# Performance work log

Hardware: AMD Instinct MI355X
Metric: run time of the kernel (lower is better)

## Reference

```python
import jax, jax.numpy as jnp
import numpy as np

B, L, D = 32, 4096, 1024

def setup_inputs() -> dict:
    key = jax.random.key(0)
    k1, k2, k3, k4 = jax.random.split(key, 4)
    doc_rep = jax.random.normal(k1, (B, L, D), dtype=jnp.float32)
    # cls_layer: Linear(input_size=D, label_size=L) -> weight [L, D], bias [L]
    W = jax.random.normal(k2, (L, D), dtype=jnp.float32) / np.sqrt(D)
    b = jax.random.normal(k3, (L,), dtype=jnp.float32) * 0.01
    # label_graph initialized as identity + learned; use identity + small noise-free eye
    G = jnp.eye(L, dtype=jnp.float32)
    return {"doc_rep": doc_rep, "W": W, "b": b, "G": G}

def reference(doc_rep, W, b, G):
    # Original computes full [B, L, L] = Linear(doc_rep) then extracts the diagonal.
    # Mathematically only the per-label dot products are needed:
    # doc_label[b, l] = doc_rep[b, l, :] @ W[l, :] + bias[l]
    doc_label = jnp.einsum('bld,ld->bl', doc_rep, W) + b  # [B, L]
    out_label = jax.nn.sigmoid(doc_label @ G)             # [B, L]
    return out_label
```

## Files before the change

### kernel.cpp

```cpp
#include <hip/hip_runtime.h>
#include <math.h>

#define BB 32
#define LL 4096
#define DD 1024
#define NCH 16
#define NJT 64
#define CTILE 256

typedef float f4 __attribute__((ext_vector_type(4)));

__global__ __launch_bounds__(256, 8) void k_dot(const float* __restrict__ doc,
                                                const float* __restrict__ W,
                                                const float* __restrict__ bias,
                                                float* __restrict__ dlT) {
  const int bid  = (blockIdx.x & 7) * 2048 + (blockIdx.x >> 3);
  const int wid  = (bid * 256 + (int)threadIdx.x) >> 6;
  const int lane = threadIdx.x & 63;
  const int b  = wid & 31;
  const int l  = (wid >> 5) << 1;

  const f4* dp = reinterpret_cast<const f4*>(doc) +
                 (((size_t)b << 20) + ((size_t)l << 8));
  const f4* wp = reinterpret_cast<const f4*>(W) + ((size_t)l << 8);

  float acc0 = 0.f, acc1 = 0.f;
  {
    f4 a0 = __builtin_nontemporal_load(&dp[lane]);
    f4 a1 = __builtin_nontemporal_load(&dp[lane + 64]);
    f4 a2 = __builtin_nontemporal_load(&dp[lane + 128]);
    f4 a3 = __builtin_nontemporal_load(&dp[lane + 192]);
    f4 w0 = wp[lane];
    f4 w1 = wp[lane + 64];
    f4 w2 = wp[lane + 128];
    f4 w3 = wp[lane + 192];
    acc0 = fmaf(a0.x, w0.x, acc0); acc0 = fmaf(a0.y, w0.y, acc0);
    acc0 = fmaf(a0.z, w0.z, acc0); acc0 = fmaf(a0.w, w0.w, acc0);
    acc0 = fmaf(a1.x, w1.x, acc0); acc0 = fmaf(a1.y, w1.y, acc0);
    acc0 = fmaf(a1.z, w1.z, acc0); acc0 = fmaf(a1.w, w1.w, acc0);
    acc0 = fmaf(a2.x, w2.x, acc0); acc0 = fmaf(a2.y, w2.y, acc0);
    acc0 = fmaf(a2.z, w2.z, acc0); acc0 = fmaf(a2.w, w2.w, acc0);
    acc0 = fmaf(a3.x, w3.x, acc0); acc0 = fmaf(a3.y, w3.y, acc0);
    acc0 = fmaf(a3.z, w3.z, acc0); acc0 = fmaf(a3.w, w3.w, acc0);
  }
  {
    f4 a0 = __builtin_nontemporal_load(&dp[lane + 256]);
    f4 a1 = __builtin_nontemporal_load(&dp[lane + 320]);
    f4 a2 = __builtin_nontemporal_load(&dp[lane + 384]);
    f4 a3 = __builtin_nontemporal_load(&dp[lane + 448]);
    f4 w0 = wp[lane + 256];
    f4 w1 = wp[lane + 320];
    f4 w2 = wp[lane + 384];
    f4 w3 = wp[lane + 448];
    acc1 = fmaf(a0.x, w0.x, acc1); acc1 = fmaf(a0.y, w0.y, acc1);
    acc1 = fmaf(a0.z, w0.z, acc1); acc1 = fmaf(a0.w, w0.w, acc1);
    acc1 = fmaf(a1.x, w1.x, acc1); acc1 = fmaf(a1.y, w1.y, acc1);
    acc1 = fmaf(a1.z, w1.z, acc1); acc1 = fmaf(a1.w, w1.w, acc1);
    acc1 = fmaf(a2.x, w2.x, acc1); acc1 = fmaf(a2.y, w2.y, acc1);
    acc1 = fmaf(a2.z, w2.z, acc1); acc1 = fmaf(a2.w, w2.w, acc1);
    acc1 = fmaf(a3.x, w3.x, acc1); acc1 = fmaf(a3.y, w3.y, acc1);
    acc1 = fmaf(a3.z, w3.z, acc1); acc1 = fmaf(a3.w, w3.w, acc1);
  }

  acc0 += __shfl_xor(acc0, 32);
  acc1 += __shfl_xor(acc1, 32);
  float c = (lane < 32) ? acc0 : acc1;
#pragma unroll
  for (int off = 16; off > 0; off >>= 1) c += __shfl_xor(c, off);

  if ((lane & 31) == 0) {
    const int row = l + (lane >> 5);
    dlT[(row << 5) + b] = c + bias[row];
  }
}

__global__ __launch_bounds__(256, 4) void k_gemm(const float* __restrict__ dlT,
                                                 const float* __restrict__ G,
                                                 float* __restrict__ part,
                                                 int chunk_l) {
  __shared__ float sdl[CTILE * BB];
  const int jt   = blockIdx.x % NJT;
  const int s    = blockIdx.x / NJT;
  const int lane = threadIdx.x & 63;
  const int w    = threadIdx.x >> 6;
  const int b0   = w << 3;
  const int j0   = (jt << 6) + lane;
  const int l0   = s * chunk_l;

  float acc[8];
#pragma unroll
  for (int b = 0; b < 8; ++b) acc[b] = 0.f;

  for (int t0 = 0; t0 < chunk_l; t0 += CTILE) {
    __syncthreads();
    {
      const float4* src = reinterpret_cast<const float4*>(dlT + (size_t)(l0 + t0) * BB);
      float4* dst = reinterpret_cast<float4*>(sdl);
#pragma unroll
      for (int k = 0; k < (CTILE * BB / 4) / 256; ++k)
        dst[k * 256 + threadIdx.x] = src[k * 256 + threadIdx.x];
    }
    __syncthreads();

    const float* gb = G + (size_t)(l0 + t0) * LL + j0;
#pragma unroll 8
    for (int il = 0; il < CTILE; ++il) {
      const float g = gb[(size_t)il * LL];
      const float4 d01 = *reinterpret_cast<const float4*>(sdl + il * BB + b0);
      const float4 d23 = *reinterpret_cast<const float4*>(sdl + il * BB + b0 + 4);
      acc[0] = fmaf(d01.x, g, acc[0]);
      acc[1] = fmaf(d01.y, g, acc[1]);
      acc[2] = fmaf(d01.z, g, acc[2]);
      acc[3] = fmaf(d01.w, g, acc[3]);
      acc[4] = fmaf(d23.x, g, acc[4]);
      acc[5] = fmaf(d23.y, g, acc[5]);
      acc[6] = fmaf(d23.z, g, acc[6]);
      acc[7] = fmaf(d23.w, g, acc[7]);
    }
  }

  float* po = part + (size_t)s * (BB * LL) + j0;
#pragma unroll
  for (int b = 0; b < 8; ++b) po[(size_t)(b0 + b) * LL] = acc[b];
}

__global__ __launch_bounds__(256) void k_reduce(const float* __restrict__ part,
                                                float* __restrict__ out,
                                                int nchunks) {
  const int i4 = blockIdx.x * 256 + threadIdx.x;
  f4 s = {0.f, 0.f, 0.f, 0.f};
  for (int c = 0; c < nchunks; ++c)
    s += *reinterpret_cast<const f4*>(part + (size_t)c * (BB * LL) + ((size_t)i4 << 2));
  f4 r;
  r.x = 1.f / (1.f + expf(-s.x));
  r.y = 1.f / (1.f + expf(-s.y));
  r.z = 1.f / (1.f + expf(-s.z));
  r.w = 1.f / (1.f + expf(-s.w));
  *reinterpret_cast<f4*>(out + ((size_t)i4 << 2)) = r;
}

extern "C" void kernel_launch(void* const* d_in, const int* in_sizes, int n_in,
                              void* d_out, int out_size, void* d_ws, size_t ws_size,
                              hipStream_t stream) {
  const float* doc  = (const float*)d_in[0];
  const float* W    = (const float*)d_in[1];
  const float* bias = (const float*)d_in[2];
  const float* G    = (const float*)d_in[3];
  float* out = (float*)d_out;

  float* dlT = (float*)d_ws;
  const size_t dl_bytes  = (size_t)BB * LL * sizeof(float);
  const size_t per_chunk = (size_t)BB * LL * sizeof(float);
  float* part = (float*)((char*)d_ws + dl_bytes);

  int nchunks = NCH;
  size_t avail = ws_size > dl_bytes ? (ws_size - dl_bytes) / per_chunk : 0;
  if ((size_t)nchunks > avail) {
    nchunks = 1;
    while ((size_t)(nchunks * 2) <= avail && nchunks * 2 <= NCH) nchunks *= 2;
  }
  const int chunk_l = LL / nchunks;

  k_dot<<<dim3((BB * LL / 2) / 4), dim3(256), 0, stream>>>(doc, W, bias, dlT);
  k_gemm<<<dim3(NJT * nchunks), dim3(256), 0, stream>>>(dlT, G, part, chunk_l);
  k_reduce<<<dim3((BB * LL / 4) / 256), dim3(256), 0, stream>>>(part, out, nchunks);
}
```

Before: 111.9 us.

## Fuse split-K reduction and sigmoid into GEMM via last-block atomic counter

Removes the separate reduce kernel. Each GEMM block writes its partial, fences, and increments a per-column-tile counter, and the last block to arrive sums all chunk partials and applies the sigmoid. The counters are zeroed inside the dot kernel. This saves one launch and lets the reduction overlap other GEMM blocks, but the last block's reads are strided scalar loads and each jt tile is serialized on one block.

```diff
diff --git a/kernel.cpp b/kernel.cpp
--- a/kernel.cpp
+++ b/kernel.cpp
@@ -13,7 +13,10 @@
 __global__ __launch_bounds__(256, 8) void k_dot(const float* __restrict__ doc,
                                                 const float* __restrict__ W,
                                                 const float* __restrict__ bias,
-                                                float* __restrict__ dlT) {
+                                                float* __restrict__ dlT,
+                                                int* __restrict__ cnt) {
+  if (blockIdx.x == 0 && threadIdx.x < NJT) cnt[threadIdx.x] = 0;
+
   const int bid  = (blockIdx.x & 7) * 2048 + (blockIdx.x >> 3);
   const int wid  = (bid * 256 + (int)threadIdx.x) >> 6;
   const int lane = threadIdx.x & 63;
@@ -77,7 +80,9 @@
 __global__ __launch_bounds__(256, 4) void k_gemm(const float* __restrict__ dlT,
                                                  const float* __restrict__ G,
                                                  float* __restrict__ part,
-                                                 int chunk_l) {
+                                                 float* __restrict__ out,
+                                                 int* __restrict__ cnt,
+                                                 int chunk_l, int nchunks) {
   __shared__ float sdl[CTILE * BB];
   const int jt   = blockIdx.x % NJT;
   const int s    = blockIdx.x / NJT;
@@ -119,24 +124,29 @@
     }
   }
 
-  float* po = part + (size_t)s * (BB * LL) + j0;
+  {
+    float* po = part + (size_t)s * (BB * LL) + j0;
 #pragma unroll
-  for (int b = 0; b < 8; ++b) po[(size_t)(b0 + b) * LL] = acc[b];
-}
+    for (int b = 0; b < 8; ++b) po[(size_t)(b0 + b) * LL] = acc[b];
+  }
 
-__global__ __launch_bounds__(256) void k_reduce(const float* __restrict__ part,
-                                                float* __restrict__ out,
-                                                int nchunks) {
-  const int i4 = blockIdx.x * 256 + threadIdx.x;
-  f4 s = {0.f, 0.f, 0.f, 0.f};
-  for (int c = 0; c < nchunks; ++c)
-    s += *reinterpret_cast<const f4*>(part + (size_t)c * (BB * LL) + ((size_t)i4 << 2));
-  f4 r;
-  r.x = 1.f / (1.f + expf(-s.x));
-  r.y = 1.f / (1.f + expf(-s.y));
-  r.z = 1.f / (1.f + expf(-s.z));
-  r.w = 1.f / (1.f + expf(-s.w));
-  *reinterpret_cast<f4*>(out + ((size_t)i4 << 2)) = r;
+  __threadfence();
+  __syncthreads();
+  __shared__ int lastFlag;
+  if (threadIdx.x == 0)
+    lastFlag = (atomicAdd(&cnt[jt], 1) == nchunks - 1);
+  __syncthreads();
+  if (lastFlag) {
+    __threadfence();
+#pragma unroll
+    for (int b = 0; b < 8; ++b) {
+      const size_t off = (size_t)(b0 + b) * LL + j0;
+      float ssum = 0.f;
+      for (int c = 0; c < nchunks; ++c)
+        ssum += part[(size_t)c * (BB * LL) + off];
+      out[off] = 1.f / (1.f + expf(-ssum));
+    }
+  }
 }
 
 extern "C" void kernel_launch(void* const* d_in, const int* in_sizes, int n_in,
@@ -154,14 +164,16 @@
   float* part = (float*)((char*)d_ws + dl_bytes);
 
   int nchunks = NCH;
-  size_t avail = ws_size > dl_bytes ? (ws_size - dl_bytes) / per_chunk : 0;
+  size_t need_cnt = NJT * sizeof(int);
+  size_t avail = ws_size > dl_bytes + need_cnt ? (ws_size - dl_bytes - need_cnt) / per_chunk : 0;
   if ((size_t)nchunks > avail) {
     nchunks = 1;
     while ((size_t)(nchunks * 2) <= avail && nchunks * 2 <= NCH) nchunks *= 2;
   }
   const int chunk_l = LL / nchunks;
+  int* cnt = (int*)((char*)d_ws + dl_bytes + (size_t)nchunks * per_chunk);
 
-  k_dot<<<dim3((BB * LL / 2) / 4), dim3(256), 0, stream>>>(doc, W, bias, dlT);
-  k_gemm<<<dim3(NJT * nchunks), dim3(256), 0, stream>>>(dlT, G, part, chunk_l);
-  k_reduce<<<dim3((BB * LL / 4) / 256), dim3(256), 0, stream>>>(part, out, nchunks);
+  k_dot<<<dim3((BB * LL / 2) / 4), dim3(256), 0, stream>>>(doc, W, bias, dlT, cnt);
+  k_gemm<<<dim3(NJT * nchunks), dim3(256), 0, stream>>>(dlT, G, part, out, cnt,
+                                                        chunk_l, nchunks);
 }
```

New measurement: 235.5 us. 2.1x slower.
